# Kernel optimization log

Measured on AMD Instinct MI355X. Metric: run time of the kernel, lower is better.

## Reference

```python
import jax, jax.numpy as jnp
import numpy as np

D_MODEL = 256
NUM_HEADS = 4
N = 2048           # num points (N == M required by the rotary theta sharing)
K_LIST = [0.5]     # per-layer top-k fraction (module's self.k)


def setup_inputs() -> dict:
    key = jax.random.key(0)
    ks = jax.random.split(key, 10)
    s = 0.05
    return {
        "input_q": jax.random.normal(ks[0], (1, N, D_MODEL), jnp.float32),
        "input_k": jax.random.normal(ks[1], (1, N, D_MODEL), jnp.float32),
        "input_v": jax.random.normal(ks[2], (1, N, D_MODEL), jnp.float32),
        "embed_qk": jax.random.normal(ks[3], (1, N, D_MODEL // 2), jnp.float32),
        "Wq": jax.random.normal(ks[4], (D_MODEL, D_MODEL), jnp.float32) * s,
        "bq": jnp.zeros((D_MODEL,), jnp.float32),
        "Wk": jax.random.normal(ks[5], (D_MODEL, D_MODEL), jnp.float32) * s,
        "bk": jnp.zeros((D_MODEL,), jnp.float32),
        "Wv": jax.random.normal(ks[6], (D_MODEL, D_MODEL), jnp.float32) * s,
        "bv": jnp.zeros((D_MODEL,), jnp.float32),
        "layer": 0,
    }


def _rotary(x, theta_half):
    # x: (b,h,n,d); theta_half: (b,h,n,d//2)
    b, h, n, d = x.shape
    xr = x.reshape(b, h, n, d // 2, 2)
    rot = jnp.stack([-xr[..., 1], xr[..., 0]], axis=-1).reshape(b, h, n, d)
    # F.interpolate(scale_factor=2, mode='nearest') == repeat each element twice
    theta = jnp.repeat(theta_half, 2, axis=-1)
    return x * jnp.cos(theta) + rot * jnp.sin(theta)


def reference(input_q, input_k, input_v, embed_qk, Wq, bq, Wk, bk, Wv, bv, layer):
    b, n, dm = input_q.shape
    h = NUM_HEADS
    dh = dm // h

    def split_heads(x):  # (b,n,dm) -> (b,h,n,dh)
        return x.reshape(b, -1, h, dh).transpose(0, 2, 1, 3)

    q = split_heads(input_q @ Wq.T + bq)
    k = split_heads(input_k @ Wk.T + bk)
    v = split_heads(input_v @ Wv.T + bv)
    theta_half = embed_qk.reshape(b, -1, h, dh // 2).transpose(0, 2, 1, 3)
    q = _rotary(q, theta_half)
    k = _rotary(k, theta_half)

    scores = jnp.einsum('bhnd,bhmd->bhnm', q, k) / jnp.sqrt(jnp.float32(dh))
    kk = int(n * K_LIST[layer])  # top-k size
    vals, idx = jax.lax.top_k(scores, kk)          # (b,h,n,kk)
    prob = jax.nn.softmax(vals, axis=-1)
    bI = jnp.arange(b)[:, None, None, None]
    hI = jnp.arange(h)[None, :, None, None]
    nI = jnp.arange(n)[None, None, :, None]
    sparse = jnp.zeros_like(scores).at[bI, hI, nI, idx].set(prob)
    hidden = jnp.einsum('bhnm,bhmd->bhnd', sparse, v)
    hidden = hidden.transpose(0, 2, 1, 3).reshape(b, n, dm)
    return hidden, sparse
```

## Files before the change

### kernel.cpp

```cpp
#include <hip/hip_runtime.h>
#include <hip/hip_bf16.h>
#include <stdint.h>

#define NPTS 2048
#define DM 256
#define NH 4
#define DH 64
#define KK 1024

#define QH_OFF 0
#define QL_OFF (NH*NPTS*DH)
#define KH_OFF (2*NH*NPTS*DH)
#define KL_OFF (3*NH*NPTS*DH)
#define VT_OFF (4*NH*NPTS*DH)

typedef __attribute__((ext_vector_type(8)))  short bf16x8;
typedef __attribute__((ext_vector_type(4)))  float f32x4;

__device__ inline ushort bf16rn(float f) {
    uint32_t u = __float_as_uint(f);
    uint32_t r = (u + 0x7FFFu + ((u >> 16) & 1u)) >> 16;
    return (ushort)r;
}
__device__ inline float bf16tof(ushort h) {
    return __uint_as_float(((uint32_t)h) << 16);
}
__device__ inline uint32_t f2u(float f) {
    uint32_t x = __float_as_uint(f);
    return (x & 0x80000000u) ? ~x : (x | 0x80000000u);
}
__device__ inline float u2f(uint32_t u) {
    uint32_t x = (u & 0x80000000u) ? (u ^ 0x80000000u) : ~u;
    return __uint_as_float(x);
}

__global__ __launch_bounds__(256) void proj_rope_kernel(
    const float* __restrict__ xq, const float* __restrict__ xk, const float* __restrict__ xv,
    const float* __restrict__ emb,
    const float* __restrict__ Wq, const float* __restrict__ bq,
    const float* __restrict__ Wk, const float* __restrict__ bk,
    const float* __restrict__ Wv, const float* __restrict__ bv,
    ushort* __restrict__ wsu)
{
    const int z = blockIdx.y;
    const int n0 = blockIdx.x * 8;
    const float* X = (z==0) ? xq : (z==1) ? xk : xv;
    const float* W = (z==0) ? Wq : (z==1) ? Wk : Wv;
    const float* B = (z==0) ? bq : (z==1) ? bk : bv;

    __shared__ float s_in[8][DM];
    {
        const float4* X4 = (const float4*)(X + (size_t)n0 * DM);
        float4* s4 = (float4*)&s_in[0][0];
        #pragma unroll
        for (int i = 0; i < 2; i++) {
            int f = threadIdx.x + 256*i;
            s4[f] = X4[f];
        }
    }
    __syncthreads();

    const int c = threadIdx.x;
    const int h = c >> 6, d = c & 63;
    const float bias = B[c];
    float acc[8];
    #pragma unroll
    for (int r = 0; r < 8; r++) acc[r] = bias;

    const float4* W4 = (const float4*)(W + (size_t)c * DM);
    #pragma unroll 4
    for (int k4 = 0; k4 < DM/4; k4++) {
        float4 w = W4[k4];
        #pragma unroll
        for (int r = 0; r < 8; r++) {
            float4 sv = *(const float4*)&s_in[r][k4*4];
            acc[r] = fmaf(sv.x, w.x, acc[r]);
            acc[r] = fmaf(sv.y, w.y, acc[r]);
            acc[r] = fmaf(sv.z, w.z, acc[r]);
            acc[r] = fmaf(sv.w, w.w, acc[r]);
        }
    }

    if (z < 2) {
        const int p = d >> 1;
        #pragma unroll
        for (int r = 0; r < 8; r++) {
            float th = emb[(size_t)(n0 + r)*(DM/2) + h*32 + p];
            float cs = cosf(th), sn = sinf(th);
            float partner = __shfl_xor(acc[r], 1);
            acc[r] = (d & 1) ? (acc[r]*cs + partner*sn) : (acc[r]*cs - partner*sn);
            if (z == 0) acc[r] *= 0.125f;
        }
        ushort* hi = wsu + ((z==0) ? QH_OFF : KH_OFF);
        ushort* lo = wsu + ((z==0) ? QL_OFF : KL_OFF);
        #pragma unroll
        for (int r = 0; r < 8; r++) {
            size_t idx = ((size_t)(h*NPTS + n0 + r))*DH + d;
            ushort hb = bf16rn(acc[r]);
            float res = acc[r] - bf16tof(hb);
            hi[idx] = hb;
            lo[idx] = bf16rn(res);
        }
    } else {
        __syncthreads();
        #pragma unroll
        for (int r = 0; r < 8; r++) s_in[r][c] = acc[r];
        __syncthreads();
        ushort tmp[8];
        #pragma unroll
        for (int r = 0; r < 8; r++) tmp[r] = bf16rn(s_in[r][c]);
        *(bf16x8*)(wsu + VT_OFF + (size_t)c*NPTS + n0) = *(bf16x8*)tmp;
    }
}

__global__ __launch_bounds__(1024, 8) void fused_attn_kernel(const ushort* __restrict__ wsu,
                                                             float* __restrict__ out)
{
    const int id = blockIdx.x;
    const int c8 = id & 7;
    const int h  = c8 >> 1;
    const int n0 = 16 * ((id >> 3) + 64 * (c8 & 1));
    float* sp = out + (size_t)NPTS*DM;
    __shared__ float LB[16384];
    char* lds = (char*)LB;

    const int w  = threadIdx.x >> 6, l = threadIdx.x & 63;
    const int cl = l & 15, cg = l >> 4;
    const uint32_t rsw = ((uint32_t)(cl & 7)) << 4;
    const uint32_t wsw = ((uint32_t)(w  & 7)) << 4;

    uint32_t u[32];

    #pragma unroll
    for (int p = 0; p < 2; p++) {
        const size_t qbase = ((size_t)(h*NPTS + n0 + cl))*DH + 8*cg;
        bf16x8 qh0 = *(const bf16x8*)(wsu + QH_OFF + qbase);
        bf16x8 qh1 = *(const bf16x8*)(wsu + QH_OFF + qbase + 32);
        bf16x8 ql0 = *(const bf16x8*)(wsu + QL_OFF + qbase);
        bf16x8 ql1 = *(const bf16x8*)(wsu + QL_OFF + qbase + 32);

        const int col0 = 1024*p + 64*w;
        #pragma unroll
        for (int t = 0; t < 4; t++) {
            const size_t kb = ((size_t)(h*NPTS + col0 + 16*t + cl))*DH + 8*cg;
            f32x4 a = {0.f, 0.f, 0.f, 0.f};
            bf16x8 ah0 = *(const bf16x8*)(wsu + KH_OFF + kb);
            bf16x8 ah1 = *(const bf16x8*)(wsu + KH_OFF + kb + 32);
            a = __builtin_amdgcn_mfma_f32_16x16x32_bf16(ah0, qh0, a, 0, 0, 0);
            a = __builtin_amdgcn_mfma_f32_16x16x32_bf16(ah1, qh1, a, 0, 0, 0);
            {
                bf16x8 al0 = *(const bf16x8*)(wsu + KL_OFF + kb);
                bf16x8 al1 = *(const bf16x8*)(wsu + KL_OFF + kb + 32);
                a = __builtin_amdgcn_mfma_f32_16x16x32_bf16(al0, qh0, a, 0, 0, 0);
                a = __builtin_amdgcn_mfma_f32_16x16x32_bf16(al1, qh1, a, 0, 0, 0);
            }
            a = __builtin_amdgcn_mfma_f32_16x16x32_bf16(ah0, ql0, a, 0, 0, 0);
            a = __builtin_amdgcn_mfma_f32_16x16x32_bf16(ah1, ql1, a, 0, 0, 0);
            uint32_t byte = (uint32_t)cl*4096u +
                ((256u*(uint32_t)w + 64u*(uint32_t)t + 16u*(uint32_t)cg) ^ rsw);
            *(f32x4*)(lds + byte) = a;
        }
        __syncthreads();
        #pragma unroll
        for (int j = 0; j < 4; j++) {
            f32x4 v = *(const f32x4*)(lds + (size_t)w*4096u +
                        ((16u*(uint32_t)(l + 64*j)) ^ wsw));
            u[16*p + 4*j + 0] = f2u(v[0]);
            u[16*p + 4*j + 1] = f2u(v[1]);
            u[16*p + 4*j + 2] = f2u(v[2]);
            u[16*p + 4*j + 3] = f2u(v[3]);
        }
        if (p == 0) __syncthreads();
    }

    uint32_t mu = 0u;
    #pragma unroll
    for (int j = 0; j < 32; j++) mu = (u[j] > mu) ? u[j] : mu;
    #pragma unroll
    for (int off = 32; off; off >>= 1) {
        uint32_t o = (uint32_t)__shfl_xor((int)mu, off);
        mu = (o > mu) ? o : mu;
    }
    const float mx = u2f(mu);

    uint32_t cur = 0u;
    for (int bit = 31; bit >= 0; bit--) {
        uint32_t cand = cur | (1u << bit);
        int c = 0;
        #pragma unroll
        for (int j = 0; j < 32; j++) c += (int)__popcll(__ballot(u[j] >= cand));
        if (c >= KK) { cur = cand; if (c == KK) break; }
    }

    float zsum = 0.f;
    #pragma unroll
    for (int j = 0; j < 32; j++) {
        bool sel = (u[j] >= cur);
        float ev = sel ? __expf(u2f(u[j]) - mx) : 0.f;
        u[j] = __float_as_uint(ev);
        zsum += ev;
    }
    #pragma unroll
    for (int off = 32; off; off >>= 1) zsum += __shfl_xor(zsum, off);
    const float rz = 1.f / zsum;

    #pragma unroll
    for (int p2 = 0; p2 < 2; p2++)
        #pragma unroll
        for (int j = 0; j < 4; j++) {
            const int b = 16*p2 + 4*j;
            float p0 = __uint_as_float(u[b+0]) * rz;
            float p1 = __uint_as_float(u[b+1]) * rz;
            float p2v = __uint_as_float(u[b+2]) * rz;
            float p3 = __uint_as_float(u[b+3]) * rz;
            uint32_t pk0 = ((uint32_t)bf16rn(p1) << 16) | (uint32_t)bf16rn(p0);
            uint32_t pk1 = ((uint32_t)bf16rn(p3) << 16) | (uint32_t)bf16rn(p2v);
            *(uint2*)(lds + (size_t)w*4096u +
                ((2048u*(uint32_t)p2 + 8u*(uint32_t)(l + 64*j)) ^ wsw)) = make_uint2(pk0, pk1);
        }
    __syncthreads();

    {
        f32x4* grow = (f32x4*)(sp + ((size_t)(h*NPTS + n0 + w))*NPTS);
        #pragma unroll
        for (int p2 = 0; p2 < 2; p2++)
            #pragma unroll
            for (int j = 0; j < 4; j++) {
                const int b = 16*p2 + 4*j;
                f32x4 pv;
                pv[0] = __uint_as_float(u[b+0]) * rz;
                pv[1] = __uint_as_float(u[b+1]) * rz;
                pv[2] = __uint_as_float(u[b+2]) * rz;
                pv[3] = __uint_as_float(u[b+3]) * rz;
                __builtin_nontemporal_store(pv, grow + 256*p2 + l + 64*j);
            }
    }

    const ushort* Vt = wsu + VT_OFF + (size_t)h*DH*NPTS;
    const int m0 = 128*w;
    f32x4 pacc[4];
    #pragma unroll
    for (int dt = 0; dt < 4; dt++) pacc[dt] = (f32x4){0.f, 0.f, 0.f, 0.f};

    #pragma unroll
    for (int s = 0; s < 4; s++) {
        const int mk = m0 + 32*s + 8*cg;
        bf16x8 bfrag = *(const bf16x8*)(lds + (size_t)cl*4096u + ((2u*(uint32_t)mk) ^ rsw));
        #pragma unroll
        for (int dt = 0; dt < 4; dt++) {
            bf16x8 afrag = *(const bf16x8*)(Vt + ((size_t)(16*dt + cl))*NPTS + mk);
            pacc[dt] = __builtin_amdgcn_mfma_f32_16x16x32_bf16(afrag, bfrag, pacc[dt], 0, 0, 0);
        }
    }
    __syncthreads();

    #pragma unroll
    for (int dt = 0; dt < 4; dt++) {
        uint32_t byte = (uint32_t)w*4096u + (uint32_t)cl*256u +
            ((64u*(uint32_t)dt + 16u*(uint32_t)cg) ^ rsw);
        *(f32x4*)(lds + byte) = pacc[dt];
    }
    __syncthreads();

    {
        const int r = w, d = l;
        const uint32_t byte = (uint32_t)r*256u +
            ((4u*(uint32_t)(d & ~3)) ^ ((uint32_t)(r & 7) << 4)) + 4u*(uint32_t)(d & 3);
        float ssum = 0.f;
        #pragma unroll
        for (int wv = 0; wv < 16; wv++)
            ssum += *(const float*)(lds + (size_t)wv*4096u + byte);
        out[(size_t)(n0 + r)*DM + h*DH + d] = ssum;
    }
}

extern "C" void kernel_launch(void* const* d_in, const int* in_sizes, int n_in,
                              void* d_out, int out_size, void* d_ws, size_t ws_size,
                              hipStream_t stream)
{
    const float* xq  = (const float*)d_in[0];
    const float* xk  = (const float*)d_in[1];
    const float* xv  = (const float*)d_in[2];
    const float* emb = (const float*)d_in[3];
    const float* Wq  = (const float*)d_in[4];
    const float* bq  = (const float*)d_in[5];
    const float* Wk  = (const float*)d_in[6];
    const float* bk  = (const float*)d_in[7];
    const float* Wv  = (const float*)d_in[8];
    const float* bv  = (const float*)d_in[9];
    float* out  = (float*)d_out;
    ushort* wsu = (ushort*)d_ws;

    proj_rope_kernel<<<dim3(NPTS/8, 3), 256, 0, stream>>>(xq, xk, xv, emb, Wq, bq, Wk, bk, Wv, bv, wsu);
    fused_attn_kernel<<<dim3(NPTS/16 * NH), 1024, 0, stream>>>(wsu, out);
}
```

Before: 102.1 us.

## Shrink attention blocks to 8 query rows with 512 threads

```diff
diff --git a/kernel.cpp b/kernel.cpp
--- a/kernel.cpp
+++ b/kernel.cpp
@@ -113,35 +113,36 @@
     }
 }
 
-__global__ __launch_bounds__(1024, 8) void fused_attn_kernel(const ushort* __restrict__ wsu,
-                                                             float* __restrict__ out)
+__global__ __launch_bounds__(512, 8) void fused_attn_kernel(const ushort* __restrict__ wsu,
+                                                            float* __restrict__ out)
 {
     const int id = blockIdx.x;
     const int c8 = id & 7;
     const int h  = c8 >> 1;
-    const int n0 = 16 * ((id >> 3) + 64 * (c8 & 1));
+    const int n0 = 8 * ((id >> 3) + 128 * (c8 & 1));
     float* sp = out + (size_t)NPTS*DM;
-    __shared__ float LB[16384];
+    __shared__ float LB[8192];
     char* lds = (char*)LB;
 
     const int w  = threadIdx.x >> 6, l = threadIdx.x & 63;
     const int cl = l & 15, cg = l >> 4;
-    const uint32_t rsw = ((uint32_t)(cl & 7)) << 4;
-    const uint32_t wsw = ((uint32_t)(w  & 7)) << 4;
+    const int qrow = cl & 7;
+    const uint32_t rsw = ((uint32_t)qrow) << 4;
+    const uint32_t wsw = ((uint32_t)w) << 4;
 
     uint32_t u[32];
 
     #pragma unroll
     for (int p = 0; p < 2; p++) {
-        const size_t qbase = ((size_t)(h*NPTS + n0 + cl))*DH + 8*cg;
+        const size_t qbase = ((size_t)(h*NPTS + n0 + qrow))*DH + 8*cg;
         bf16x8 qh0 = *(const bf16x8*)(wsu + QH_OFF + qbase);
         bf16x8 qh1 = *(const bf16x8*)(wsu + QH_OFF + qbase + 32);
         bf16x8 ql0 = *(const bf16x8*)(wsu + QL_OFF + qbase);
         bf16x8 ql1 = *(const bf16x8*)(wsu + QL_OFF + qbase + 32);
 
-        const int col0 = 1024*p + 64*w;
-        #pragma unroll
-        for (int t = 0; t < 4; t++) {
+        const int col0 = 1024*p + 128*w;
+        #pragma unroll
+        for (int t = 0; t < 8; t++) {
             const size_t kb = ((size_t)(h*NPTS + col0 + 16*t + cl))*DH + 8*cg;
             f32x4 a = {0.f, 0.f, 0.f, 0.f};
             bf16x8 ah0 = *(const bf16x8*)(wsu + KH_OFF + kb);
@@ -156,9 +157,11 @@
             }
             a = __builtin_amdgcn_mfma_f32_16x16x32_bf16(ah0, ql0, a, 0, 0, 0);
             a = __builtin_amdgcn_mfma_f32_16x16x32_bf16(ah1, ql1, a, 0, 0, 0);
-            uint32_t byte = (uint32_t)cl*4096u +
-                ((256u*(uint32_t)w + 64u*(uint32_t)t + 16u*(uint32_t)cg) ^ rsw);
-            *(f32x4*)(lds + byte) = a;
+            if (cl < 8) {
+                uint32_t byte = (uint32_t)qrow*4096u +
+                    ((512u*(uint32_t)w + 64u*(uint32_t)t + 16u*(uint32_t)cg) ^ rsw);
+                *(f32x4*)(lds + byte) = a;
+            }
         }
         __syncthreads();
         #pragma unroll
@@ -203,22 +206,6 @@
     #pragma unroll
     for (int off = 32; off; off >>= 1) zsum += __shfl_xor(zsum, off);
     const float rz = 1.f / zsum;
-
-    #pragma unroll
-    for (int p2 = 0; p2 < 2; p2++)
-        #pragma unroll
-        for (int j = 0; j < 4; j++) {
-            const int b = 16*p2 + 4*j;
-            float p0 = __uint_as_float(u[b+0]) * rz;
-            float p1 = __uint_as_float(u[b+1]) * rz;
-            float p2v = __uint_as_float(u[b+2]) * rz;
-            float p3 = __uint_as_float(u[b+3]) * rz;
-            uint32_t pk0 = ((uint32_t)bf16rn(p1) << 16) | (uint32_t)bf16rn(p0);
-            uint32_t pk1 = ((uint32_t)bf16rn(p3) << 16) | (uint32_t)bf16rn(p2v);
-            *(uint2*)(lds + (size_t)w*4096u +
-                ((2048u*(uint32_t)p2 + 8u*(uint32_t)(l + 64*j)) ^ wsw)) = make_uint2(pk0, pk1);
-        }
-    __syncthreads();
 
     {
         f32x4* grow = (f32x4*)(sp + ((size_t)(h*NPTS + n0 + w))*NPTS);
@@ -232,20 +219,25 @@
                 pv[1] = __uint_as_float(u[b+1]) * rz;
                 pv[2] = __uint_as_float(u[b+2]) * rz;
                 pv[3] = __uint_as_float(u[b+3]) * rz;
+                uint32_t pk0 = ((uint32_t)bf16rn(pv[1]) << 16) | (uint32_t)bf16rn(pv[0]);
+                uint32_t pk1 = ((uint32_t)bf16rn(pv[3]) << 16) | (uint32_t)bf16rn(pv[2]);
+                *(uint2*)(lds + (size_t)w*4096u +
+                    ((2048u*(uint32_t)p2 + 8u*(uint32_t)(l + 64*j)) ^ wsw)) = make_uint2(pk0, pk1);
                 __builtin_nontemporal_store(pv, grow + 256*p2 + l + 64*j);
             }
     }
+    __syncthreads();
 
     const ushort* Vt = wsu + VT_OFF + (size_t)h*DH*NPTS;
-    const int m0 = 128*w;
+    const int m0 = 256*w;
     f32x4 pacc[4];
     #pragma unroll
     for (int dt = 0; dt < 4; dt++) pacc[dt] = (f32x4){0.f, 0.f, 0.f, 0.f};
 
     #pragma unroll
-    for (int s = 0; s < 4; s++) {
+    for (int s = 0; s < 8; s++) {
         const int mk = m0 + 32*s + 8*cg;
-        bf16x8 bfrag = *(const bf16x8*)(lds + (size_t)cl*4096u + ((2u*(uint32_t)mk) ^ rsw));
+        bf16x8 bfrag = *(const bf16x8*)(lds + (size_t)qrow*4096u + ((2u*(uint32_t)mk) ^ rsw));
         #pragma unroll
         for (int dt = 0; dt < 4; dt++) {
             bf16x8 afrag = *(const bf16x8*)(Vt + ((size_t)(16*dt + cl))*NPTS + mk);
@@ -254,22 +246,24 @@
     }
     __syncthreads();
 
-    #pragma unroll
-    for (int dt = 0; dt < 4; dt++) {
-        uint32_t byte = (uint32_t)w*4096u + (uint32_t)cl*256u +
-            ((64u*(uint32_t)dt + 16u*(uint32_t)cg) ^ rsw);
-        *(f32x4*)(lds + byte) = pacc[dt];
+    if (cl < 8) {
+        #pragma unroll
+        for (int dt = 0; dt < 4; dt++) {
+            uint32_t byte = (uint32_t)w*2048u + (uint32_t)cl*256u +
+                ((64u*(uint32_t)dt + 16u*(uint32_t)cg) ^ rsw);
+            *(f32x4*)(lds + byte) = pacc[dt];
+        }
     }
     __syncthreads();
 
     {
-        const int r = w, d = l;
+        const int r = threadIdx.x >> 6, d = threadIdx.x & 63;
         const uint32_t byte = (uint32_t)r*256u +
-            ((4u*(uint32_t)(d & ~3)) ^ ((uint32_t)(r & 7) << 4)) + 4u*(uint32_t)(d & 3);
+            ((4u*(uint32_t)(d & ~3)) ^ ((uint32_t)r << 4)) + 4u*(uint32_t)(d & 3);
         float ssum = 0.f;
         #pragma unroll
-        for (int wv = 0; wv < 16; wv++)
-            ssum += *(const float*)(lds + (size_t)wv*4096u + byte);
+        for (int wv = 0; wv < 8; wv++)
+            ssum += *(const float*)(lds + (size_t)wv*2048u + byte);
         out[(size_t)(n0 + r)*DM + h*DH + d] = ssum;
     }
 }
@@ -292,5 +286,5 @@
     ushort* wsu = (ushort*)d_ws;
 
     proj_rope_kernel<<<dim3(NPTS/8, 3), 256, 0, stream>>>(xq, xk, xv, emb, Wq, bq, Wk, bk, Wv, bv, wsu);
-    fused_attn_kernel<<<dim3(NPTS/16 * NH), 1024, 0, stream>>>(wsu, out);
-}
+    fused_attn_kernel<<<dim3(NPTS/8 * NH), 512, 0, stream>>>(wsu, out);
+}
```

Measured after the change: 138.6 us. 35.8% more time.

## Keep half of score row in LDS to cut register pressure in top-k

Applied to the files above, without the earlier changes.

```diff
diff --git a/kernel.cpp b/kernel.cpp
--- a/kernel.cpp
+++ b/kernel.cpp
@@ -16,6 +16,7 @@
 
 typedef __attribute__((ext_vector_type(8)))  short bf16x8;
 typedef __attribute__((ext_vector_type(4)))  float f32x4;
+typedef __attribute__((ext_vector_type(4)))  uint  u32x4;
 
 __device__ inline ushort bf16rn(float f) {
     uint32_t u = __float_as_uint(f);
@@ -113,7 +114,7 @@
     }
 }
 
-__global__ __launch_bounds__(1024, 8) void fused_attn_kernel(const ushort* __restrict__ wsu,
+__global__ __launch_bounds__(1024, 4) void fused_attn_kernel(const ushort* __restrict__ wsu,
                                                              float* __restrict__ out)
 {
     const int id = blockIdx.x;
@@ -128,8 +129,9 @@
     const int cl = l & 15, cg = l >> 4;
     const uint32_t rsw = ((uint32_t)(cl & 7)) << 4;
     const uint32_t wsw = ((uint32_t)(w  & 7)) << 4;
-
-    uint32_t u[32];
+    char* myrow = lds + (size_t)w*4096u;
+
+    uint32_t u[16];
 
     #pragma unroll
     for (int p = 0; p < 2; p++) {
@@ -161,21 +163,29 @@
             *(f32x4*)(lds + byte) = a;
         }
         __syncthreads();
-        #pragma unroll
-        for (int j = 0; j < 4; j++) {
-            f32x4 v = *(const f32x4*)(lds + (size_t)w*4096u +
-                        ((16u*(uint32_t)(l + 64*j)) ^ wsw));
-            u[16*p + 4*j + 0] = f2u(v[0]);
-            u[16*p + 4*j + 1] = f2u(v[1]);
-            u[16*p + 4*j + 2] = f2u(v[2]);
-            u[16*p + 4*j + 3] = f2u(v[3]);
-        }
-        if (p == 0) __syncthreads();
+        if (p == 0) {
+            #pragma unroll
+            for (int j = 0; j < 4; j++) {
+                f32x4 v = *(const f32x4*)(myrow + ((16u*(uint32_t)(l + 64*j)) ^ wsw));
+                u[4*j+0] = f2u(v[0]); u[4*j+1] = f2u(v[1]);
+                u[4*j+2] = f2u(v[2]); u[4*j+3] = f2u(v[3]);
+            }
+            __syncthreads();
+        }
     }
 
     uint32_t mu = 0u;
     #pragma unroll
-    for (int j = 0; j < 32; j++) mu = (u[j] > mu) ? u[j] : mu;
+    for (int j = 0; j < 4; j++) {
+        uint32_t byte = (16u*(uint32_t)(l + 64*j)) ^ wsw;
+        f32x4 v = *(const f32x4*)(myrow + byte);
+        u32x4 kv;
+        #pragma unroll
+        for (int i = 0; i < 4; i++) { kv[i] = f2u(v[i]); mu = (kv[i] > mu) ? kv[i] : mu; }
+        *(u32x4*)(myrow + byte) = kv;
+    }
+    #pragma unroll
+    for (int j = 0; j < 16; j++) mu = (u[j] > mu) ? u[j] : mu;
     #pragma unroll
     for (int off = 32; off; off >>= 1) {
         uint32_t o = (uint32_t)__shfl_xor((int)mu, off);
@@ -188,53 +198,92 @@
         uint32_t cand = cur | (1u << bit);
         int c = 0;
         #pragma unroll
-        for (int j = 0; j < 32; j++) c += (int)__popcll(__ballot(u[j] >= cand));
+        for (int j = 0; j < 16; j++) c += (int)__popcll(__ballot(u[j] >= cand));
+        #pragma unroll
+        for (int j = 0; j < 4; j++) {
+            u32x4 kv = *(const u32x4*)(myrow + ((16u*(uint32_t)(l + 64*j)) ^ wsw));
+            #pragma unroll
+            for (int i = 0; i < 4; i++) c += (int)__popcll(__ballot(kv[i] >= cand));
+        }
         if (c >= KK) { cur = cand; if (c == KK) break; }
     }
 
     float zsum = 0.f;
     #pragma unroll
-    for (int j = 0; j < 32; j++) {
-        bool sel = (u[j] >= cur);
-        float ev = sel ? __expf(u2f(u[j]) - mx) : 0.f;
-        u[j] = __float_as_uint(ev);
-        zsum += ev;
+    for (int j = 0; j < 16; j++)
+        if (u[j] >= cur) zsum += __expf(u2f(u[j]) - mx);
+    #pragma unroll
+    for (int j = 0; j < 4; j++) {
+        u32x4 kv = *(const u32x4*)(myrow + ((16u*(uint32_t)(l + 64*j)) ^ wsw));
+        #pragma unroll
+        for (int i = 0; i < 4; i++)
+            if (kv[i] >= cur) zsum += __expf(u2f(kv[i]) - mx);
     }
     #pragma unroll
     for (int off = 32; off; off >>= 1) zsum += __shfl_xor(zsum, off);
     const float rz = 1.f / zsum;
 
     #pragma unroll
-    for (int p2 = 0; p2 < 2; p2++)
-        #pragma unroll
-        for (int j = 0; j < 4; j++) {
-            const int b = 16*p2 + 4*j;
-            float p0 = __uint_as_float(u[b+0]) * rz;
-            float p1 = __uint_as_float(u[b+1]) * rz;
-            float p2v = __uint_as_float(u[b+2]) * rz;
-            float p3 = __uint_as_float(u[b+3]) * rz;
-            uint32_t pk0 = ((uint32_t)bf16rn(p1) << 16) | (uint32_t)bf16rn(p0);
-            uint32_t pk1 = ((uint32_t)bf16rn(p3) << 16) | (uint32_t)bf16rn(p2v);
-            *(uint2*)(lds + (size_t)w*4096u +
-                ((2048u*(uint32_t)p2 + 8u*(uint32_t)(l + 64*j)) ^ wsw)) = make_uint2(pk0, pk1);
-        }
+    for (int j = 0; j < 16; j++) {
+        float ev = (u[j] >= cur) ? __expf(u2f(u[j]) - mx) * rz : 0.f;
+        u[j] = __float_as_uint(ev);
+    }
+
+    float pr2[8], plow[8];
+    f32x4* grow4 = (f32x4*)(sp + ((size_t)(h*NPTS + n0 + w))*NPTS);
+    #pragma unroll
+    for (int j = 0; j < 2; j++) {
+        u32x4 kv = *(const u32x4*)(myrow + ((2048u + 16u*(uint32_t)(l + 64*j)) ^ wsw));
+        #pragma unroll
+        for (int i = 0; i < 4; i++)
+            pr2[4*j+i] = (kv[i] >= cur) ? __expf(u2f(kv[i]) - mx) * rz : 0.f;
+    }
+    #pragma unroll
+    for (int j = 0; j < 2; j++) {
+        uint32_t pk0 = ((uint32_t)bf16rn(pr2[4*j+1]) << 16) | (uint32_t)bf16rn(pr2[4*j+0]);
+        uint32_t pk1 = ((uint32_t)bf16rn(pr2[4*j+3]) << 16) | (uint32_t)bf16rn(pr2[4*j+2]);
+        *(uint2*)(myrow + ((3072u + 8u*(uint32_t)(l + 64*j)) ^ wsw)) = make_uint2(pk0, pk1);
+    }
+    #pragma unroll
+    for (int j = 0; j < 2; j++) {
+        u32x4 kv = *(const u32x4*)(myrow + ((16u*(uint32_t)(l + 64*j)) ^ wsw));
+        #pragma unroll
+        for (int i = 0; i < 4; i++)
+            plow[4*j+i] = (kv[i] >= cur) ? __expf(u2f(kv[i]) - mx) * rz : 0.f;
+    }
+    #pragma unroll
+    for (int j = 0; j < 2; j++) {
+        uint32_t pk0 = ((uint32_t)bf16rn(plow[4*j+1]) << 16) | (uint32_t)bf16rn(plow[4*j+0]);
+        uint32_t pk1 = ((uint32_t)bf16rn(plow[4*j+3]) << 16) | (uint32_t)bf16rn(plow[4*j+2]);
+        *(uint2*)(myrow + ((2048u + 8u*(uint32_t)(l + 64*j)) ^ wsw)) = make_uint2(pk0, pk1);
+    }
+    #pragma unroll
+    for (int j = 0; j < 4; j++) {
+        uint32_t pk0 = ((uint32_t)bf16rn(__uint_as_float(u[4*j+1])) << 16)
+                     | (uint32_t)bf16rn(__uint_as_float(u[4*j+0]));
+        uint32_t pk1 = ((uint32_t)bf16rn(__uint_as_float(u[4*j+3])) << 16)
+                     | (uint32_t)bf16rn(__uint_as_float(u[4*j+2]));
+        *(uint2*)(myrow + ((8u*(uint32_t)(l + 64*j)) ^ wsw)) = make_uint2(pk0, pk1);
+    }
+
+    #pragma unroll
+    for (int j = 0; j < 4; j++) {
+        f32x4 pv;
+        pv[0] = __uint_as_float(u[4*j+0]); pv[1] = __uint_as_float(u[4*j+1]);
+        pv[2] = __uint_as_float(u[4*j+2]); pv[3] = __uint_as_float(u[4*j+3]);
+        __builtin_nontemporal_store(pv, grow4 + l + 64*j);
+    }
+    #pragma unroll
+    for (int j = 0; j < 2; j++) {
+        f32x4 pv; pv[0] = plow[4*j+0]; pv[1] = plow[4*j+1]; pv[2] = plow[4*j+2]; pv[3] = plow[4*j+3];
+        __builtin_nontemporal_store(pv, grow4 + 256 + l + 64*j);
+    }
+    #pragma unroll
+    for (int j = 0; j < 2; j++) {
+        f32x4 pv; pv[0] = pr2[4*j+0]; pv[1] = pr2[4*j+1]; pv[2] = pr2[4*j+2]; pv[3] = pr2[4*j+3];
+        __builtin_nontemporal_store(pv, grow4 + 384 + l + 64*j);
+    }
     __syncthreads();
-
-    {
-        f32x4* grow = (f32x4*)(sp + ((size_t)(h*NPTS + n0 + w))*NPTS);
-        #pragma unroll
-        for (int p2 = 0; p2 < 2; p2++)
-            #pragma unroll
-            for (int j = 0; j < 4; j++) {
-                const int b = 16*p2 + 4*j;
-                f32x4 pv;
-                pv[0] = __uint_as_float(u[b+0]) * rz;
-                pv[1] = __uint_as_float(u[b+1]) * rz;
-                pv[2] = __uint_as_float(u[b+2]) * rz;
-                pv[3] = __uint_as_float(u[b+3]) * rz;
-                __builtin_nontemporal_store(pv, grow + 256*p2 + l + 64*j);
-            }
-    }
 
     const ushort* Vt = wsu + VT_OFF + (size_t)h*DH*NPTS;
     const int m0 = 128*w;
@@ -263,7 +312,7 @@
     __syncthreads();
 
     {
-        const int r = w, d = l;
+        const int r = threadIdx.x >> 6, d = threadIdx.x & 63;
         const uint32_t byte = (uint32_t)r*256u +
             ((4u*(uint32_t)(d & ~3)) ^ ((uint32_t)(r & 7) << 4)) + 4u*(uint32_t)(d & 3);
         float ssum = 0.f;
```

New measurement: 117.6 us. 15.2% more time.
